# Kernel optimization log

Measured on AMD Instinct MI355X. Metric: run time of the kernel, lower is better.

## Reference

```python
import jax, jax.numpy as jnp
import numpy as np

H = 32; L = 4; HEADS = 8; VC = 16; BIG = 1e9

def _unit(v):
    return v * jax.lax.rsqrt(jnp.sum(v * v, -1, keepdims=True) + 1e-8)

def _dihedrals(bb):
    n = bb.shape[0]
    X = bb[:, :3].reshape(n * 3, 3)
    U = _unit(X[1:] - X[:-1])
    u2, u1, u0 = U[:-2], U[1:-1], U[2:]
    n2 = _unit(jnp.cross(u2, u1)); n1 = _unit(jnp.cross(u1, u0))
    cosD = jnp.clip(jnp.sum(n2 * n1, -1), -1 + 1e-6, 1 - 1e-6)
    D = jnp.sign(jnp.sum(u2 * n1, -1)) * jnp.arccos(cosD)
    D = jnp.pad(D, (1, 2)).reshape(n, 3)
    return jnp.concatenate([jnp.cos(D), jnp.sin(D)], -1)

def _orientations(x):
    f = jnp.pad(_unit(x[1:] - x[:-1]), ((0, 1), (0, 0)))
    b = jnp.pad(_unit(x[:-1] - x[1:]), ((1, 0), (0, 0)))
    return jnp.stack([f, b], -2)

def _virtual_cb(bb):
    n_, ca, c = bb[:, 0], bb[:, 1], bb[:, 2]
    b = ca - n_; cc = c - ca; a = jnp.cross(b, cc)
    return -0.58273431 * a + 0.56802827 * b - 0.54067466 * cc + ca

def _rbf(d, nbin=16, dmax=20.0):
    mu = jnp.linspace(0.0, dmax, nbin); sig = dmax / nbin
    return jnp.exp(-(((d[..., None] - mu) / sig) ** 2))

def _pos_emb(didx, nemb=16):
    freq = jnp.exp(jnp.arange(0, nemb, 2, dtype=jnp.float32) * (-np.log(10000.0) / nemb))
    ang = didx[..., None].astype(jnp.float32) * freq
    return jnp.concatenate([jnp.cos(ang), jnp.sin(ang)], -1)

def _edge_rot(vec):
    # per-edge rotation aligning edge direction to e_y (equiformer-style)
    nrm = _unit(vec)
    helper = jnp.where(jnp.abs(nrm[..., 2:3]) > 0.99, jnp.array([1.0, 0.0, 0.0]), jnp.array([0.0, 0.0, 1.0]))
    z = _unit(jnp.cross(nrm, helper))
    x = jnp.cross(nrm, z)
    return jnp.stack([x, nrm, z], axis=-2)

def _rot(R, x):
    return jnp.concatenate([x[..., :1, :], jnp.einsum('...ij,...jc->...ic', R, x[..., 1:, :])], -2)

def _rot_inv(R, x):
    return jnp.concatenate([x[..., :1, :], jnp.einsum('...ji,...jc->...ic', R, x[..., 1:, :])], -2)

def _norm_so3(x, g0, b0, g1):
    x0 = x[..., 0, :]; x1 = x[..., 1:, :]
    mu = jnp.mean(x0, -1, keepdims=True)
    var = jnp.var(x0, -1, keepdims=True)
    y0 = (x0 - mu) * jax.lax.rsqrt(var + 1e-6) * g0 + b0
    y1 = x1 * jax.lax.rsqrt(jnp.mean(x1 * x1, (-2, -1), keepdims=True) + 1e-6) * g1
    return jnp.concatenate([y0[..., None, :], y1], -2)

def _project(xin, nbr, R, ef, rw1, rw2, ow):
    src = _rot(R, xin[nbr])                         # [N,k,4,Cin] gather + rotate into edge frame
    rad = jax.nn.silu(ef @ rw1) @ rw2               # [N,k,Cin] radial weights
    msg = _rot_inv(R, src * rad[..., None, :])      # rotate back to global frame
    return jnp.mean(msg, axis=1) @ ow               # [N,4,Cout]

def _forward(bb, latent, ln_g0, ln_b0, ln_g1, bb_rad_w1, bb_rad_w2, bb_out_w,
             lat_rad_w1, lat_rad_w2, lat_out_w, tln_g0, tln_b0, tln_g1,
             attn_w1, attn_w2, v_w, o_w, ffn_w1, ffn_w2, ffn_wg, ffn_v1,
             eu_w1, eu_w2, out_rad_w1, out_rad_w2, out_w,
             seq_w1, seq_b1, seq_w2, seq_b2, seq_w3, seq_b3, x_mask, n_per, k):
    N = bb.shape[0]
    Xca = bb[:, 1]
    # backbone SO3 features [N,4,7]: l=0 dihedrals (padded to 7), l=1 seven vectors
    dih = jnp.pad(_dihedrals(bb), ((0, 0), (0, 1)))
    vecs = jnp.concatenate([bb - Xca[:, None], _orientations(Xca),
                            (_virtual_cb(bb) - Xca)[:, None]], -2)
    bb_feat = jnp.concatenate([dih[:, None, :], jnp.nan_to_num(jnp.swapaxes(vecs, -1, -2))], 1)
    # kNN graph within each chain; masked residues pushed far away
    batch = jnp.arange(N) // n_per
    mx = jnp.where(x_mask[:, None], BIG, Xca)
    sq = jnp.sum(mx * mx, -1)
    d2 = sq[:, None] + sq[None, :] - 2.0 * (mx @ mx.T)
    bad = (batch[:, None] != batch[None, :]) | jnp.eye(N, dtype=bool)
    d2 = jnp.where(bad, BIG, d2)
    _, nbr = jax.lax.top_k(-d2, k)                  # [N,k] source indices per target
    edge_vec = Xca[:, None] - Xca[nbr]
    R = _edge_rot(edge_vec)                         # [N,k,3,3]
    dist = jnp.sqrt(jnp.sum(edge_vec * edge_vec, -1) + 1e-12)
    ef = jnp.concatenate([_rbf(dist), _pos_emb(nbr - jnp.arange(N)[:, None])], -1)  # [N,k,32]
    lat = _norm_so3(latent, ln_g0, ln_b0, ln_g1)
    x = jnp.concatenate([_project(bb_feat, nbr, R, ef, bb_rad_w1, bb_rad_w2, bb_out_w),
                         _project(lat, nbr, R, ef, lat_rad_w1, lat_rad_w2, lat_out_w)], -1)  # [N,4,H]
    for l in range(L):
        xl = _norm_so3(x, tln_g0[l], tln_b0[l], tln_g1[l])
        src = xl[nbr]                               # [N,k,4,H]
        feat = jnp.concatenate([src[..., 0, :],
                                jnp.broadcast_to(xl[:, None, 0, :], src[..., 0, :].shape),
                                ef], -1)            # [N,k,3H]
        alpha = jax.nn.softmax(jax.nn.silu(feat @ attn_w1[l]) @ attn_w2[l], axis=1)  # [N,k,heads]
        v = _rot_inv(R, _rot(R, src) @ v_w[l])      # [N,k,4,heads*vc]
        v = v.reshape(N, k, 4, HEADS, VC)
        agg = jnp.einsum('nkh,nkchv->nchv', alpha, v).reshape(N, 4, HEADS * VC)
        x = x + agg @ o_w[l]
        h = jax.nn.silu(x[:, 0, :] @ ffn_w1[l])
        gate = jax.nn.sigmoid(h @ ffn_wg[l])
        x = x + jnp.concatenate([(h @ ffn_w2[l])[:, None, :],
                                 (x[:, 1:, :] @ ffn_v1[l]) * gate[:, None, :]], 1)
        e_in = jnp.concatenate([ef, x[nbr][..., 0, :],
                                jnp.broadcast_to(x[:, None, 0, :], (N, k, H))], -1)
        ef = ef + jax.nn.silu(e_in @ eu_w1[l]) @ eu_w2[l]
    atoms = _project(x, nbr, R, ef, out_rad_w1, out_rad_w2, out_w)  # [N,4,91]
    decoded_latent = jnp.swapaxes(atoms[:, 1:4, :], -1, -2)         # [N,91,3]
    hh = jax.nn.relu(x[:, 0, :] @ seq_w1 + seq_b1)
    hh = jax.nn.relu(hh @ seq_w2 + seq_b2)
    seq_logits = jax.nn.log_softmax(hh @ seq_w3 + seq_b3, -1)
    return decoded_latent, seq_logits

def setup_inputs() -> dict:
    key = jax.random.key(0)
    N = 8192; n_per = 2048; k = 30
    keys = iter(jax.random.split(key, 64))
    def W(shape):
        fan = shape[-2] if len(shape) > 1 else shape[-1]
        return (jax.random.normal(next(keys), shape) / np.sqrt(fan)).astype(jnp.float32)
    inp = {
        'bb': (jax.random.normal(next(keys), (N, 4, 3)) * 3.0).astype(jnp.float32),
        'latent': jax.random.normal(next(keys), (N, 4, H), dtype=jnp.float32),
        'ln_g0': jnp.ones((H,), jnp.float32), 'ln_b0': jnp.zeros((H,), jnp.float32), 'ln_g1': jnp.ones((H,), jnp.float32),
        'bb_rad_w1': W((H, 64)), 'bb_rad_w2': W((64, 7)), 'bb_out_w': W((7, 16)),
        'lat_rad_w1': W((H, 64)), 'lat_rad_w2': W((64, H)), 'lat_out_w': W((H, 16)),
        'tln_g0': jnp.ones((L, H), jnp.float32), 'tln_b0': jnp.zeros((L, H), jnp.float32), 'tln_g1': jnp.ones((L, H), jnp.float32),
        'attn_w1': W((L, 3 * H, H)), 'attn_w2': W((L, H, HEADS)),
        'v_w': W((L, H, HEADS * VC)), 'o_w': W((L, HEADS * VC, H)),
        'ffn_w1': W((L, H, 2 * H)), 'ffn_w2': W((L, 2 * H, H)), 'ffn_wg': W((L, 2 * H, H)), 'ffn_v1': W((L, H, H)),
        'eu_w1': W((L, 3 * H, 2 * H)), 'eu_w2': W((L, 2 * H, H)),
        'out_rad_w1': W((H, 64)), 'out_rad_w2': W((64, H)), 'out_w': W((H, 91)),
        'seq_w1': W((H, 64)), 'seq_b1': jnp.zeros((64,), jnp.float32),
        'seq_w2': W((64, H)), 'seq_b2': jnp.zeros((H,), jnp.float32),
        'seq_w3': W((H, 20)), 'seq_b3': jnp.zeros((20,), jnp.float32),
        'x_mask': jnp.zeros((N,), bool), 'n_per': n_per, 'k': k,
    }
    return inp

def reference(bb, latent, ln_g0, ln_b0, ln_g1, bb_rad_w1, bb_rad_w2, bb_out_w,
              lat_rad_w1, lat_rad_w2, lat_out_w, tln_g0, tln_b0, tln_g1,
              attn_w1, attn_w2, v_w, o_w, ffn_w1, ffn_w2, ffn_wg, ffn_v1,
              eu_w1, eu_w2, out_rad_w1, out_rad_w2, out_w,
              seq_w1, seq_b1, seq_w2, seq_b2, seq_w3, seq_b3, x_mask, n_per, k):
    return _forward(bb, latent, ln_g0, ln_b0, ln_g1, bb_rad_w1, bb_rad_w2, bb_out_w,
                    lat_rad_w1, lat_rad_w2, lat_out_w, tln_g0, tln_b0, tln_g1,
                    attn_w1, attn_w2, v_w, o_w, ffn_w1, ffn_w2, ffn_wg, ffn_v1,
                    eu_w1, eu_w2, out_rad_w1, out_rad_w2, out_w,
                    seq_w1, seq_b1, seq_w2, seq_b2, seq_w3, seq_b3, x_mask, n_per, k)
```

## Files before the change

### kernel.cpp

```cpp
#include <hip/hip_runtime.h>
#include <math.h>

#define NRES 8192
#define NPER 2048
#define KNB  30
#define NEDGE (NRES*KNB)

__device__ __forceinline__ float siluf(float x){ return x / (1.0f + __expf(-x)); }

__global__ void k_bbfeat(const float* __restrict__ bb, float* __restrict__ bbf,
                         float4* __restrict__ ca){
  int n = blockIdx.x*256 + threadIdx.x;
  if(n >= NRES) return;
  const float* r = bb + n*12;
  float cax=r[3], cay=r[4], caz=r[5];
  ca[n] = make_float4(cax,cay,caz, cax*cax+cay*cay+caz*caz);
  float vx[7],vy[7],vz[7];
  for(int a=0;a<4;a++){ vx[a]=r[a*3]-cax; vy[a]=r[a*3+1]-cay; vz[a]=r[a*3+2]-caz; }
  if(n<NRES-1){
    float dx=bb[(n+1)*12+3]-cax, dy=bb[(n+1)*12+4]-cay, dz=bb[(n+1)*12+5]-caz;
    float s=rsqrtf(dx*dx+dy*dy+dz*dz+1e-8f);
    vx[4]=dx*s; vy[4]=dy*s; vz[4]=dz*s;
  } else { vx[4]=0.f; vy[4]=0.f; vz[4]=0.f; }
  if(n>0){
    float dx=bb[(n-1)*12+3]-cax, dy=bb[(n-1)*12+4]-cay, dz=bb[(n-1)*12+5]-caz;
    float s=rsqrtf(dx*dx+dy*dy+dz*dz+1e-8f);
    vx[5]=dx*s; vy[5]=dy*s; vz[5]=dz*s;
  } else { vx[5]=0.f; vy[5]=0.f; vz[5]=0.f; }
  {
    float bx=cax-r[0], by=cay-r[1], bz=caz-r[2];
    float cx=r[6]-cax, cy=r[7]-cay, cz=r[8]-caz;
    float axx=by*cz-bz*cy, ayy=bz*cx-bx*cz, azz=bx*cy-by*cx;
    vx[6]=-0.58273431f*axx+0.56802827f*bx-0.54067466f*cx;
    vy[6]=-0.58273431f*ayy+0.56802827f*by-0.54067466f*cy;
    vz[6]=-0.58273431f*azz+0.56802827f*bz-0.54067466f*cz;
  }
  float cD[3], sD[3];
  for(int t=0;t<3;t++){
    cD[t]=1.0f; sD[t]=0.0f;
    int f=3*n+t-1;
    if(f>=0 && f<3*NRES-3){
      float X[4][3];
      for(int q=0;q<4;q++){
        int m=f+q, rr=m/3, aa=m-rr*3;
        X[q][0]=bb[rr*12+aa*3]; X[q][1]=bb[rr*12+aa*3+1]; X[q][2]=bb[rr*12+aa*3+2];
      }
      float u2x=X[1][0]-X[0][0], u2y=X[1][1]-X[0][1], u2z=X[1][2]-X[0][2];
      float u1x=X[2][0]-X[1][0], u1y=X[2][1]-X[1][1], u1z=X[2][2]-X[1][2];
      float u0x=X[3][0]-X[2][0], u0y=X[3][1]-X[2][1], u0z=X[3][2]-X[2][2];
      float s2=rsqrtf(u2x*u2x+u2y*u2y+u2z*u2z+1e-8f); u2x*=s2; u2y*=s2; u2z*=s2;
      float s1=rsqrtf(u1x*u1x+u1y*u1y+u1z*u1z+1e-8f); u1x*=s1; u1y*=s1; u1z*=s1;
      float s0=rsqrtf(u0x*u0x+u0y*u0y+u0z*u0z+1e-8f); u0x*=s0; u0y*=s0; u0z*=s0;
      float n2x=u2y*u1z-u2z*u1y, n2y=u2z*u1x-u2x*u1z, n2z=u2x*u1y-u2y*u1x;
      float nn2=rsqrtf(n2x*n2x+n2y*n2y+n2z*n2z+1e-8f); n2x*=nn2; n2y*=nn2; n2z*=nn2;
      float n1x=u1y*u0z-u1z*u0y, n1y=u1z*u0x-u1x*u0z, n1z=u1x*u0y-u1y*u0x;
      float nn1=rsqrtf(n1x*n1x+n1y*n1y+n1z*n1z+1e-8f); n1x*=nn1; n1y*=nn1; n1z*=nn1;
      float dotn = n2x*n1x+n2y*n1y+n2z*n1z;
      float cosD = fminf(fmaxf(dotn, -1.0f+1e-6f), 1.0f-1e-6f);
      float sg = u2x*n1x+u2y*n1y+u2z*n1z;
      if(sg==0.0f){ cD[t]=1.0f; sD[t]=0.0f; }
      else {
        float sgn = (sg>0.0f)?1.0f:-1.0f;
        cD[t]=cosD;
        sD[t]=sgn*sqrtf(fmaxf(1.0f-cosD*cosD,0.0f));
      }
    }
  }
  float* o = bbf + n*28;
  o[0]=cD[0]; o[1]=cD[1]; o[2]=cD[2]; o[3]=sD[0]; o[4]=sD[1]; o[5]=sD[2]; o[6]=0.f;
  for(int c=0;c<7;c++){ o[7+c]=vx[c]; o[14+c]=vy[c]; o[21+c]=vz[c]; }
}

__global__ __launch_bounds__(256) void k_knn(const float4* __restrict__ ca, int* __restrict__ nbr){
  __shared__ float sx[NPER], sy[NPER], sz[NPER], sq[NPER];
  int wave = threadIdx.x>>6;
  int lane = threadIdx.x&63;
  int i = blockIdx.x*4 + wave;
  int batch = i / NPER;
  int base = batch*NPER;
  for(int t=threadIdx.x; t<NPER; t+=256){
    float4 c = ca[base+t];
    sx[t]=c.x; sy[t]=c.y; sz[t]=c.z; sq[t]=c.w;
  }
  __syncthreads();
  int il = i - base;
  float xi=sx[il], yi=sy[il], zi=sz[il], si=sq[il];
  float vals[32];
  float lmin = 1e30f; int larg = 0;
  #pragma unroll
  for(int t=0;t<32;t++){
    int j = t*64 + lane;
    float d2 = si + sq[j] - 2.0f*(xi*sx[j]+yi*sy[j]+zi*sz[j]);
    if(j==il) d2 = 1e30f;
    vals[t]=d2;
    if(d2 < lmin){ lmin=d2; larg=t; }
  }
  for(int it=0; it<KNB; it++){
    float v = lmin; int jg = larg*64 + lane;
    #pragma unroll
    for(int off=32; off>0; off>>=1){
      float vo = __shfl_xor(v, off, 64);
      int   jo = __shfl_xor(jg, off, 64);
      if(vo < v || (vo==v && jo<jg)){ v=vo; jg=jo; }
    }
    if(lane==0) nbr[i*KNB+it] = base + jg;
    if((jg&63)==lane){
      int targ = jg>>6;
      lmin = 1e30f; larg = 0;
      #pragma unroll
      for(int t=0;t<32;t++){
        if(t==targ) vals[t]=1e30f;
        if(vals[t]<lmin){ lmin=vals[t]; larg=t; }
      }
    }
  }
}

__global__ void k_tbl(float* __restrict__ tbl){
  int i = blockIdx.x*256 + threadIdx.x;
  int d = i>>3, m = i&7;
  float freq = __expf(-1.1512925465f*(float)m);
  float ang = (float)(d-2048)*freq;
  tbl[d*16+m]   = cosf(ang);
  tbl[d*16+8+m] = sinf(ang);
}

__global__ void k_edgefeat(const float4* __restrict__ ca, const int* __restrict__ nbr,
                           const float* __restrict__ tbl, float* __restrict__ ef){
  int e = blockIdx.x*256 + threadIdx.x;
  if(e >= NEDGE) return;
  int n = e/KNB;
  int j = nbr[e];
  float4 cn = ca[n], cj = ca[j];
  float dx=cn.x-cj.x, dy=cn.y-cj.y, dz=cn.z-cj.z;
  float dist = sqrtf(dx*dx+dy*dy+dz*dz + 1e-12f);
  float f[32];
  #pragma unroll
  for(int m=0;m<16;m++){
    float mu = (20.0f/15.0f)*(float)m;
    float t = (dist-mu)*(1.0f/1.25f);
    f[m] = __expf(-t*t);
  }
  {
    const float4* t4 = (const float4*)(tbl + (size_t)(j - n + 2048)*16);
    float4 c0=t4[0], c1=t4[1], s0=t4[2], s1=t4[3];
    f[16]=c0.x; f[17]=c0.y; f[18]=c0.z; f[19]=c0.w;
    f[20]=c1.x; f[21]=c1.y; f[22]=c1.z; f[23]=c1.w;
    f[24]=s0.x; f[25]=s0.y; f[26]=s0.z; f[27]=s0.w;
    f[28]=s1.x; f[29]=s1.y; f[30]=s1.z; f[31]=s1.w;
  }
  float4* o4 = (float4*)(ef + (size_t)e*32);
  #pragma unroll
  for(int q=0;q<8;q++) o4[q] = make_float4(f[q*4],f[q*4+1],f[q*4+2],f[q*4+3]);
}

__global__ void k_norm(const float* __restrict__ in, float* __restrict__ out,
                       const float* __restrict__ g0, const float* __restrict__ b0,
                       const float* __restrict__ g1){
  int tid = blockIdx.x*256 + threadIdx.x;
  int n = tid >> 5, lane = tid & 31;
  if(n >= NRES) return;
  const float* xn = in + n*128;
  float x0 = xn[lane];
  float s = x0, s2 = x0*x0;
  for(int off=16; off>0; off>>=1){ s += __shfl_xor(s, off, 32); s2 += __shfl_xor(s2, off, 32); }
  float mu = s*(1.0f/32.0f);
  float var = s2*(1.0f/32.0f) - mu*mu;
  float y0 = (x0-mu)*rsqrtf(var+1e-6f)*g0[lane] + b0[lane];
  float v1 = xn[32+lane], v2 = xn[64+lane], v3 = xn[96+lane];
  float ss = v1*v1+v2*v2+v3*v3;
  for(int off=16; off>0; off>>=1){ ss += __shfl_xor(ss, off, 32); }
  float sc = rsqrtf(ss*(1.0f/96.0f) + 1e-6f);
  float g = g1[lane];
  out[n*128+lane]     = y0;
  out[n*128+32+lane]  = v1*sc*g;
  out[n*128+64+lane]  = v2*sc*g;
  out[n*128+96+lane]  = v3*sc*g;
}

__device__ __forceinline__ void load32(float* __restrict__ f, const float* __restrict__ src){
  const float4* s4 = (const float4*)src;
  #pragma unroll
  for(int q=0;q<8;q++){
    float4 v = s4[q];
    f[q*4+0]=v.x; f[q*4+1]=v.y; f[q*4+2]=v.z; f[q*4+3]=v.w;
  }
}

__global__ __launch_bounds__(128) __attribute__((amdgpu_waves_per_eu(4,4)))
void k_rad(const float* __restrict__ ef,
           const float* __restrict__ bbw1, const float* __restrict__ bbw2,
           const float* __restrict__ latw1, const float* __restrict__ latw2,
           float* __restrict__ radbb, float* __restrict__ radlat){
  int e = blockIdx.x*128 + threadIdx.x;
  float f[32];
  load32(f, ef + (size_t)e*32);
  float ab[7];
  #pragma unroll
  for(int t=0;t<7;t++) ab[t]=0.f;
  #pragma unroll
  for(int half=0; half<2; half++){
    float h[32];
    #pragma unroll
    for(int o=0;o<32;o++) h[o]=0.f;
    #pragma unroll
    for(int c=0;c<32;c++){
      const float* w = bbw1 + c*64 + half*32;
      #pragma unroll
      for(int o=0;o<32;o++) h[o] += f[c]*w[o];
    }
    #pragma unroll
    for(int o=0;o<32;o++){
      float v = siluf(h[o]);
      const float* w2 = bbw2 + (half*32+o)*7;
      #pragma unroll
      for(int t=0;t<7;t++) ab[t] += v*w2[t];
    }
  }
  {
    float4* rb4 = (float4*)(radbb + (size_t)e*8);
    rb4[0] = make_float4(ab[0],ab[1],ab[2],ab[3]);
    rb4[1] = make_float4(ab[4],ab[5],ab[6],0.f);
  }
  float al[32];
  #pragma unroll
  for(int t=0;t<32;t++) al[t]=0.f;
  #pragma unroll
  for(int half=0; half<2; half++){
    float h[32];
    #pragma unroll
    for(int o=0;o<32;o++) h[o]=0.f;
    #pragma unroll
    for(int c=0;c<32;c++){
      const float* w = latw1 + c*64 + half*32;
      #pragma unroll
      for(int o=0;o<32;o++) h[o] += f[c]*w[o];
    }
    #pragma unroll
    for(int o=0;o<32;o++){
      float v = siluf(h[o]);
      const float* w2 = latw2 + (half*32+o)*32;
      #pragma unroll
      for(int t=0;t<32;t++) al[t] += v*w2[t];
    }
  }
  float4* rl4 = (float4*)(radlat + (size_t)e*32);
  #pragma unroll
  for(int q=0;q<8;q++) rl4[q] = make_float4(al[q*4],al[q*4+1],al[q*4+2],al[q*4+3]);
}

__global__ __launch_bounds__(256) void k_init(const int* __restrict__ nbr,
                       const float* __restrict__ radbb, const float* __restrict__ radlat,
                       const float* __restrict__ bbf, const float* __restrict__ latn,
                       const float* __restrict__ bboutw, const float* __restrict__ latoutw,
                       const float* __restrict__ g0, const float* __restrict__ b0,
                       const float* __restrict__ g1,
                       float* __restrict__ x, float* __restrict__ xl){
  __shared__ float msgbb[4][32], msglat[4][128], xout[4][128];
  int g = threadIdx.x>>6, t = threadIdx.x&63;
  int n = blockIdx.x*4 + g;
  int t31 = t&31, t7 = t%7;
  float accL0=0.f, accL1=0.f, accB=0.f;
  for(int kk=0; kk<KNB; kk++){
    int e = n*KNB+kk;
    int j = nbr[e];
    float rl = radlat[(size_t)e*32 + t31];
    accL0 += latn[j*128+t]    * rl;
    accL1 += latn[j*128+64+t] * rl;
    if(t<28) accB += bbf[j*28+t]*radbb[(size_t)e*8 + t7];
  }
  msglat[g][t]=accL0*(1.0f/KNB); msglat[g][64+t]=accL1*(1.0f/KNB);
  if(t<28) msgbb[g][t]=accB*(1.0f/KNB);
  for(int half=0; half<2; half++){
    int e = half*64+t;
    int rrow = e>>5, c = e&31;
    float v=0.f;
    if(c<16){ for(int q=0;q<7;q++)  v += msgbb[g][rrow*7+q]*bboutw[q*16+c]; }
    else    { for(int q=0;q<32;q++) v += msglat[g][rrow*32+q]*latoutw[q*16+(c-16)]; }
    xout[g][e]=v;
    x[n*128+e]=v;
  }
  if(t<32){
    float x0=xout[g][t];
    float s=x0, s2=x0*x0;
    for(int off=16; off>0; off>>=1){ s+=__shfl_xor(s,off,32); s2+=__shfl_xor(s2,off,32); }
    float mu=s*(1.0f/32.0f), var=s2*(1.0f/32.0f)-mu*mu;
    float y0=(x0-mu)*rsqrtf(var+1e-6f)*g0[t]+b0[t];
    float v1=xout[g][32+t], v2=xout[g][64+t], v3=xout[g][96+t];
    float ss=v1*v1+v2*v2+v3*v3;
    for(int off=16; off>0; off>>=1) ss+=__shfl_xor(ss,off,32);
    float sc=rsqrtf(ss*(1.0f/96.0f)+1e-6f);
    float gg=g1[t];
    xl[n*128+t]=y0; xl[n*128+32+t]=v1*sc*gg; xl[n*128+64+t]=v2*sc*gg; xl[n*128+96+t]=v3*sc*gg;
  }
}

__global__ __launch_bounds__(256) void k_nodeprep(const float* __restrict__ x,
                       const float* __restrict__ xl,
                       const float* __restrict__ ew1, const float* __restrict__ aw1,
                       float* __restrict__ hsrc, float* __restrict__ hdst,
                       float* __restrict__ asrc, float* __restrict__ adst){
  __shared__ float sx[4][32], sl[4][32];
  int g = threadIdx.x>>6, lane = threadIdx.x&63;
  int n = blockIdx.x*4 + g;
  if(lane<32){
    if(x)   sx[g][lane] = x[n*128+lane];
    if(aw1) sl[g][lane] = xl[n*128+lane];
  }
  __syncthreads();
  if(x){
    float a0=0.f, a1=0.f;
    #pragma unroll
    for(int c=0;c<32;c++){
      float xv = sx[g][c];
      a0 += xv*ew1[(32+c)*64+lane];
      a1 += xv*ew1[(64+c)*64+lane];
    }
    hsrc[n*64+lane]=a0; hdst[n*64+lane]=a1;
  }
  if(aw1){
    int o = lane&31;
    int roff = (lane>=32)? 32 : 0;
    float a=0.f;
    #pragma unroll
    for(int c=0;c<32;c++) a += sl[g][c]*aw1[(roff+c)*32+o];
    if(lane<32) asrc[n*32+o]=a; else adst[n*32+o]=a;
  }
}

__global__ __launch_bounds__(128) __attribute__((amdgpu_waves_per_eu(4,4)))
void k_logits(const int* __restrict__ nbr,
              const float* __restrict__ asrc, const float* __restrict__ adst,
              const float* __restrict__ ef, const float* __restrict__ w1,
              const float* __restrict__ w2, float* __restrict__ logits){
  int e = blockIdx.x*128 + threadIdx.x;
  int n = e/KNB;
  int j = nbr[e];
  float h[32];
  {
    const float4* pj = (const float4*)(asrc + (size_t)j*32);
    const float4* pn = (const float4*)(adst + (size_t)n*32);
    #pragma unroll
    for(int q=0;q<8;q++){
      float4 a = pj[q], b = pn[q];
      h[q*4+0]=a.x+b.x; h[q*4+1]=a.y+b.y; h[q*4+2]=a.z+b.z; h[q*4+3]=a.w+b.w;
    }
  }
  float f[32];
  load32(f, ef + (size_t)e*32);
  #pragma unroll
  for(int c=0;c<32;c++){
    const float* w = w1 + (64+c)*32;
    #pragma unroll
    for(int o=0;o<32;o++) h[o] += f[c]*w[o];
  }
  float acc[8];
  #pragma unroll
  for(int t=0;t<8;t++) acc[t]=0.f;
  #pragma unroll
  for(int o=0;o<32;o++){
    float v = siluf(h[o]);
    const float* w = w2 + o*8;
    #pragma unroll
    for(int t=0;t<8;t++) acc[t] += v*w[t];
  }
  float4* lg4 = (float4*)(logits + (size_t)e*8);
  lg4[0] = make_float4(acc[0],acc[1],acc[2],acc[3]);
  lg4[1] = make_float4(acc[4],acc[5],acc[6],acc[7]);
}

__global__ __launch_bounds__(256) void k_update(const int* __restrict__ nbr, const float* __restrict__ xl,
                         const float* __restrict__ logits, float* __restrict__ x,
                         float* __restrict__ xlout,
                         const float* __restrict__ vw, const float* __restrict__ ow,
                         const float* __restrict__ fw1, const float* __restrict__ fw2,
                         const float* __restrict__ fwg, const float* __restrict__ fv1,
                         const float* __restrict__ g0, const float* __restrict__ b0,
                         const float* __restrict__ g1){
  __shared__ float S_lg[4][240], S_m[4][8], S_inv[4][8];
  __shared__ float S_S[4][1024], S_agg[4][512], S_x[4][128];
  __shared__ float S_h[4][64], S_g[4][32], S_d0[4][32];
  int g = threadIdx.x>>6, t = threadIdx.x&63;
  int n = blockIdx.x*4 + g;
  for(int r=t; r<240; r+=64) S_lg[g][r] = logits[(size_t)n*240+r];
  if(t<8){
    float m=-1e30f;
    for(int kk=0;kk<KNB;kk++) m=fmaxf(m, S_lg[g][kk*8+t]);
    float s=0.f;
    for(int kk=0;kk<KNB;kk++) s += __expf(S_lg[g][kk*8+t]-m);
    S_m[g][t]=m; S_inv[g][t]=1.0f/s;
  }
  for(int r=t; r<240; r+=64){ int h=r&7; S_lg[g][r]=__expf(S_lg[g][r]-S_m[g][h])*S_inv[g][h]; }
  int hd = t>>3, i8 = t&7;
  const float4* xl4 = (const float4*)xl;
  float acc[16];
  for(int m=0;m<16;m++) acc[m]=0.f;
  for(int kk=0;kk<KNB;kk++){
    int j=nbr[n*KNB+kk];
    float a = S_lg[g][kk*8+hd];
    float4 b0v = xl4[j*32 + i8*4 + 0];
    float4 b1v = xl4[j*32 + i8*4 + 1];
    float4 b2v = xl4[j*32 + i8*4 + 2];
    float4 b3v = xl4[j*32 + i8*4 + 3];
    acc[0]+=a*b0v.x; acc[1]+=a*b0v.y; acc[2]+=a*b0v.z; acc[3]+=a*b0v.w;
    acc[4]+=a*b1v.x; acc[5]+=a*b1v.y; acc[6]+=a*b1v.z; acc[7]+=a*b1v.w;
    acc[8]+=a*b2v.x; acc[9]+=a*b2v.y; acc[10]+=a*b2v.z; acc[11]+=a*b2v.w;
    acc[12]+=a*b3v.x; acc[13]+=a*b3v.y; acc[14]+=a*b3v.z; acc[15]+=a*b3v.w;
  }
  for(int m=0;m<16;m++) S_S[g][hd*128 + i8*16 + m] = acc[m];
  for(int half=0; half<2; half++){
    int hv = half*64+t;
    int hh = hv>>4;
    float a0=0.f,a1=0.f,a2=0.f,a3=0.f;
    for(int c=0;c<32;c++){
      float w = vw[c*128+hv];
      a0 += S_S[g][hh*128 + c]*w;
      a1 += S_S[g][hh*128 + 32+c]*w;
      a2 += S_S[g][hh*128 + 64+c]*w;
      a3 += S_S[g][hh*128 + 96+c]*w;
    }
    S_agg[g][hv]=a0; S_agg[g][128+hv]=a1; S_agg[g][256+hv]=a2; S_agg[g][384+hv]=a3;
  }
  for(int half=0; half<2; half++){
    int e = half*64+t;
    int rrow = e>>5, c = e&31;
    float v = x[n*128+e];
    for(int hv=0;hv<128;hv++) v += S_agg[g][rrow*128+hv]*ow[hv*32+c];
    S_x[g][e]=v;
  }
  {
    float hs=0.f;
    for(int c=0;c<32;c++) hs += S_x[g][c]*fw1[c*64+t];
    S_h[g][t]=siluf(hs);
  }
  if(t<32){
    float gs=0.f, d0=0.f;
    for(int c=0;c<64;c++){ float hv=S_h[g][c]; gs += hv*fwg[c*32+t]; d0 += hv*fw2[c*32+t]; }
    S_g[g][t]=1.0f/(1.0f+__expf(-gs));
    S_d0[g][t]=d0;
  }
  for(int half=0; half<2; half++){
    int e = half*64+t;
    int rrow = e>>5, c = e&31;
    float xv = S_x[g][e], outv;
    if(rrow==0){ outv = xv + S_d0[g][c]; }
    else {
      float dv=0.f;
      for(int cc=0;cc<32;cc++) dv += S_x[g][rrow*32+cc]*fv1[cc*32+c];
      outv = xv + dv*S_g[g][c];
    }
    S_x[g][e]=outv;
    x[n*128+e]=outv;
  }
  if(t<32){
    float x0=S_x[g][t];
    float s=x0, s2=x0*x0;
    for(int off=16; off>0; off>>=1){ s+=__shfl_xor(s,off,32); s2+=__shfl_xor(s2,off,32); }
    float mu=s*(1.0f/32.0f), var=s2*(1.0f/32.0f)-mu*mu;
    float y0=(x0-mu)*rsqrtf(var+1e-6f)*g0[t]+b0[t];
    float v1=S_x[g][32+t], v2=S_x[g][64+t], v3=S_x[g][96+t];
    float ss=v1*v1+v2*v2+v3*v3;
    for(int off=16; off>0; off>>=1) ss+=__shfl_xor(ss,off,32);
    float sc=rsqrtf(ss*(1.0f/96.0f)+1e-6f);
    float gg=g1[t];
    xlout[n*128+t]=y0; xlout[n*128+32+t]=v1*sc*gg;
    xlout[n*128+64+t]=v2*sc*gg; xlout[n*128+96+t]=v3*sc*gg;
  }
}

template<bool FUSE_LOGITS>
__global__ __launch_bounds__(128) __attribute__((amdgpu_waves_per_eu(4,4)))
void k_efup_t(const int* __restrict__ nbr,
              const float* __restrict__ hsrc, const float* __restrict__ hdst,
              const float* __restrict__ ew1, const float* __restrict__ ew2,
              float* __restrict__ ef,
              const float* __restrict__ asrc, const float* __restrict__ adst,
              const float* __restrict__ aw1n, const float* __restrict__ aw2n,
              float* __restrict__ logits){
  int e = blockIdx.x*128 + threadIdx.x;
  int n = e/KNB;
  int j = nbr[e];
  float f[32];
  load32(f, ef + (size_t)e*32);
  float acc[32];
  #pragma unroll
  for(int t=0;t<32;t++) acc[t]=0.f;
  #pragma unroll
  for(int half=0; half<2; half++){
    float h[32];
    {
      const float4* pj = (const float4*)(hsrc + (size_t)j*64 + half*32);
      const float4* pn = (const float4*)(hdst + (size_t)n*64 + half*32);
      #pragma unroll
      for(int q=0;q<8;q++){
        float4 a = pj[q], b = pn[q];
        h[q*4+0]=a.x+b.x; h[q*4+1]=a.y+b.y; h[q*4+2]=a.z+b.z; h[q*4+3]=a.w+b.w;
      }
    }
    #pragma unroll
    for(int c=0;c<32;c++){
      const float* w = ew1 + c*64 + half*32;
      #pragma unroll
      for(int o=0;o<32;o++) h[o] += f[c]*w[o];
    }
    #pragma unroll
    for(int o=0;o<32;o++){
      float v = siluf(h[o]);
      const float* w2 = ew2 + (half*32+o)*32;
      #pragma unroll
      for(int t=0;t<32;t++) acc[t] += v*w2[t];
    }
  }
  #pragma unroll
  for(int t=0;t<32;t++) f[t] += acc[t];
  float4* e4 = (float4*)(ef + (size_t)e*32);
  #pragma unroll
  for(int q=0;q<8;q++)
    e4[q] = make_float4(f[q*4+0], f[q*4+1], f[q*4+2], f[q*4+3]);
  if(FUSE_LOGITS){
    float h2[32];
    {
      const float4* pj = (const float4*)(asrc + (size_t)j*32);
      const float4* pn = (const float4*)(adst + (size_t)n*32);
      #pragma unroll
      for(int q=0;q<8;q++){
        float4 a = pj[q], b = pn[q];
        h2[q*4+0]=a.x+b.x; h2[q*4+1]=a.y+b.y; h2[q*4+2]=a.z+b.z; h2[q*4+3]=a.w+b.w;
      }
    }
    #pragma unroll
    for(int c=0;c<32;c++){
      const float* w = aw1n + (64+c)*32;
      #pragma unroll
      for(int o=0;o<32;o++) h2[o] += f[c]*w[o];
    }
    float a8[8];
    #pragma unroll
    for(int t=0;t<8;t++) a8[t]=0.f;
    #pragma unroll
    for(int o=0;o<32;o++){
      float v = siluf(h2[o]);
      const float* w = aw2n + o*8;
      #pragma unroll
      for(int t=0;t<8;t++) a8[t] += v*w[t];
    }
    float4* lg4 = (float4*)(logits + (size_t)e*8);
    lg4[0] = make_float4(a8[0],a8[1],a8[2],a8[3]);
    lg4[1] = make_float4(a8[4],a8[5],a8[6],a8[7]);
  }
}

__global__ __launch_bounds__(128) __attribute__((amdgpu_waves_per_eu(4,4)))
void k_orad(const float* __restrict__ ef,
            const float* __restrict__ orw1, const float* __restrict__ orw2,
            float* __restrict__ orad){
  int e = blockIdx.x*128 + threadIdx.x;
  float f[32];
  load32(f, ef + (size_t)e*32);
  float acc[32];
  #pragma unroll
  for(int t=0;t<32;t++) acc[t]=0.f;
  #pragma unroll
  for(int half=0; half<2; half++){
    float h[32];
    #pragma unroll
    for(int o=0;o<32;o++) h[o]=0.f;
    #pragma unroll
    for(int c=0;c<32;c++){
      const float* w = orw1 + c*64 + half*32;
      #pragma unroll
      for(int o=0;o<32;o++) h[o] += f[c]*w[o];
    }
    #pragma unroll
    for(int o=0;o<32;o++){
      float v = siluf(h[o]);
      const float* w2 = orw2 + (half*32+o)*32;
      #pragma unroll
      for(int t=0;t<32;t++) acc[t] += v*w2[t];
    }
  }
  float4* r4 = (float4*)(orad + (size_t)e*32);
  #pragma unroll
  for(int q=0;q<8;q++) r4[q] = make_float4(acc[q*4],acc[q*4+1],acc[q*4+2],acc[q*4+3]);
}

__global__ __launch_bounds__(256) void k_out(const int* __restrict__ nbr, const float* __restrict__ orad,
                      const float* __restrict__ x,
                      const float* __restrict__ outw,
                      const float* __restrict__ sw1, const float* __restrict__ sb1,
                      const float* __restrict__ sw2, const float* __restrict__ sb2,
                      const float* __restrict__ sw3, const float* __restrict__ sb3,
                      float* __restrict__ out, float* __restrict__ outseq){
  __shared__ float msg[4][128];
  __shared__ float h1[4][64], h2[4][32], lgs[4][20];
  int g = threadIdx.x>>6, t = threadIdx.x&63;
  int n = blockIdx.x*4 + g;
  int t31 = t&31;
  float acc0=0.f, acc1=0.f;
  for(int kk=0;kk<KNB;kk++){
    int e=n*KNB+kk;
    int j=nbr[e];
    float rl = orad[(size_t)e*32 + t31];
    acc0 += x[j*128+t]*rl;
    acc1 += x[j*128+64+t]*rl;
  }
  msg[g][t]=acc0*(1.0f/KNB); msg[g][64+t]=acc1*(1.0f/KNB);
  for(int o=t;o<91;o+=64){
    for(int rrow=1;rrow<4;rrow++){
      float s=0.f;
      for(int c=0;c<32;c++) s += msg[g][rrow*32+c]*outw[c*91+o];
      out[(size_t)n*273 + o*3 + (rrow-1)] = s;
    }
  }
  {
    float s=0.f;
    for(int c=0;c<32;c++) s += x[n*128+c]*sw1[c*64+t];
    h1[g][t]=fmaxf(s+sb1[t],0.f);
  }
  if(t<32){
    float s=0.f;
    for(int c=0;c<64;c++) s += h1[g][c]*sw2[c*32+t];
    h2[g][t]=fmaxf(s+sb2[t],0.f);
  }
  if(t<20){
    float s=0.f;
    for(int c=0;c<32;c++) s += h2[g][c]*sw3[c*20+t];
    lgs[g][t]=s+sb3[t];
  }
  if(t<20){
    float m=-1e30f;
    for(int c=0;c<20;c++) m=fmaxf(m,lgs[g][c]);
    float se=0.f;
    for(int c=0;c<20;c++) se += __expf(lgs[g][c]-m);
    outseq[(size_t)n*20+t]=lgs[g][t]-m-logf(se);
  }
}

extern "C" void kernel_launch(void* const* d_in, const int* in_sizes, int n_in,
                              void* d_out, int out_size, void* d_ws, size_t ws_size,
                              hipStream_t stream) {
  const float* bb      = (const float*)d_in[0];
  const float* latent  = (const float*)d_in[1];
  const float* ln_g0   = (const float*)d_in[2];
  const float* ln_b0   = (const float*)d_in[3];
  const float* ln_g1   = (const float*)d_in[4];
  const float* bbw1    = (const float*)d_in[5];
  const float* bbw2    = (const float*)d_in[6];
  const float* bboutw  = (const float*)d_in[7];
  const float* latw1   = (const float*)d_in[8];
  const float* latw2   = (const float*)d_in[9];
  const float* latoutw = (const float*)d_in[10];
  const float* tg0     = (const float*)d_in[11];
  const float* tb0     = (const float*)d_in[12];
  const float* tg1     = (const float*)d_in[13];
  const float* aw1     = (const float*)d_in[14];
  const float* aw2     = (const float*)d_in[15];
  const float* vw      = (const float*)d_in[16];
  const float* ow      = (const float*)d_in[17];
  const float* fw1     = (const float*)d_in[18];
  const float* fw2     = (const float*)d_in[19];
  const float* fwg     = (const float*)d_in[20];
  const float* fv1     = (const float*)d_in[21];
  const float* ew1     = (const float*)d_in[22];
  const float* ew2     = (const float*)d_in[23];
  const float* orw1    = (const float*)d_in[24];
  const float* orw2    = (const float*)d_in[25];
  const float* outw    = (const float*)d_in[26];
  const float* sw1     = (const float*)d_in[27];
  const float* sb1     = (const float*)d_in[28];
  const float* sw2     = (const float*)d_in[29];
  const float* sb2     = (const float*)d_in[30];
  const float* sw3     = (const float*)d_in[31];
  const float* sb3     = (const float*)d_in[32];
  float* outp = (float*)d_out;

  int*    nbr    = (int*)d_ws;
  float*  ef     = (float*)((char*)d_ws + 1024*1024);
  float*  xbuf   = ef   + (size_t)NEDGE*32;
  float*  xlA    = xbuf + (size_t)NRES*128;
  float*  xlB    = xlA  + (size_t)NRES*128;
  float*  bbf    = xlB  + (size_t)NRES*128;
  float*  logits = bbf  + (size_t)NRES*28;
  float4* ca     = (float4*)(logits + (size_t)NEDGE*8);
  float*  edgescratch = (float*)(ca + NRES);
  float*  radbb  = logits;
  float*  radlat = edgescratch;
  float*  orad   = edgescratch;
  float*  tbl    = edgescratch;
  float*  hsrc   = edgescratch;
  float*  hdst   = edgescratch + (size_t)NRES*64;
  float*  asrc   = edgescratch + (size_t)NRES*128;
  float*  adst   = edgescratch + (size_t)NRES*128 + (size_t)NRES*32;

  k_bbfeat  <<<NRES/256, 256, 0, stream>>>(bb, bbf, ca);
  k_knn     <<<NRES/4,   256, 0, stream>>>(ca, nbr);
  k_tbl     <<<4096*8/256, 256, 0, stream>>>(tbl);
  k_edgefeat<<<NEDGE/256, 256, 0, stream>>>(ca, nbr, tbl, ef);
  k_norm    <<<NRES*32/256, 256, 0, stream>>>(latent, xlA, ln_g0, ln_b0, ln_g1);
  k_rad     <<<NEDGE/128, 128, 0, stream>>>(ef, bbw1, bbw2, latw1, latw2, radbb, radlat);
  k_init    <<<NRES/4, 256, 0, stream>>>(nbr, radbb, radlat, bbf, xlA,
                                         bboutw, latoutw,
                                         tg0, tb0, tg1,
                                         xbuf, xlB);
  k_nodeprep<<<NRES/4, 256, 0, stream>>>(nullptr, xlB, ew1, aw1, hsrc, hdst, asrc, adst);
  k_logits  <<<NEDGE/128, 128, 0, stream>>>(nbr, asrc, adst, ef, aw1, aw2, logits);
  for(int l=0;l<4;l++){
    const float* xl_in  = (l&1) ? xlA : xlB;
    float*       xl_out = (l&1) ? xlB : xlA;
    int ln = (l+1<4) ? (l+1) : 3;
    k_update <<<NRES/4, 256, 0, stream>>>(nbr, xl_in, logits, xbuf, xl_out,
                                          vw+l*32*128, ow+l*128*32,
                                          fw1+l*32*64, fw2+l*64*32,
                                          fwg+l*64*32, fv1+l*32*32,
                                          tg0+ln*32, tb0+ln*32, tg1+ln*32);
    if(l<3){
      k_nodeprep<<<NRES/4, 256, 0, stream>>>(xbuf, xl_out, ew1+l*96*64, aw1+(l+1)*96*32,
                                             hsrc, hdst, asrc, adst);
      k_efup_t<true><<<NEDGE/128, 128, 0, stream>>>(nbr, hsrc, hdst,
                                                    ew1+l*96*64, ew2+l*64*32, ef,
                                                    asrc, adst,
                                                    aw1+(l+1)*96*32, aw2+(l+1)*32*8, logits);
    } else {
      k_nodeprep<<<NRES/4, 256, 0, stream>>>(xbuf, xl_out, ew1+l*96*64, nullptr,
                                             hsrc, hdst, asrc, adst);
      k_efup_t<false><<<NEDGE/128, 128, 0, stream>>>(nbr, hsrc, hdst,
                                                     ew1+l*96*64, ew2+l*64*32, ef,
                                                     nullptr, nullptr,
                                                     nullptr, nullptr, nullptr);
    }
  }
  k_orad<<<NEDGE/128, 128, 0, stream>>>(ef, orw1, orw2, orad);
  k_out <<<NRES/4, 256, 0, stream>>>(nbr, orad, xbuf, outw,
                                     sw1, sb1, sw2, sb2, sw3, sb3,
                                     outp, outp + (size_t)NRES*273);
}
```

Baseline: 1.147 ms.

## Pack edge MLPs into float2 vectors, rework kNN selection, adjust update syncs

```diff
diff --git a/kernel.cpp b/kernel.cpp
--- a/kernel.cpp
+++ b/kernel.cpp
@@ -6,7 +6,10 @@
 #define KNB  30
 #define NEDGE (NRES*KNB)
 
+typedef float v2f __attribute__((ext_vector_type(2)));
+
 __device__ __forceinline__ float siluf(float x){ return x / (1.0f + __expf(-x)); }
+__device__ __forceinline__ v2f splat2(float a){ v2f r; r.x=a; r.y=a; return r; }
 
 __global__ void k_bbfeat(const float* __restrict__ bb, float* __restrict__ bbf,
                          float4* __restrict__ ca){
@@ -71,6 +74,19 @@
   for(int c=0;c<7;c++){ o[7+c]=vx[c]; o[14+c]=vy[c]; o[21+c]=vz[c]; }
 }
 
+__device__ __forceinline__ unsigned long long knn_extract(const float* __restrict__ vals,
+                                                          unsigned &mask, int lane){
+  float bm=INFINITY; int ba=0;
+  #pragma unroll
+  for(int t=0;t<32;t++){
+    if(!((mask>>t)&1u) && vals[t]<bm){ bm=vals[t]; ba=t; }
+  }
+  mask |= 1u<<ba;
+  unsigned ub = __float_as_uint(bm);
+  ub ^= (ub & 0x80000000u) ? 0xFFFFFFFFu : 0x80000000u;
+  return ((unsigned long long)ub<<32) | (unsigned)(ba*64+lane);
+}
+
 __global__ __launch_bounds__(256) void k_knn(const float4* __restrict__ ca, int* __restrict__ nbr){
   __shared__ float sx[NPER], sy[NPER], sz[NPER], sq[NPER];
   int wave = threadIdx.x>>6;
@@ -86,32 +102,30 @@
   int il = i - base;
   float xi=sx[il], yi=sy[il], zi=sz[il], si=sq[il];
   float vals[32];
-  float lmin = 1e30f; int larg = 0;
   #pragma unroll
   for(int t=0;t<32;t++){
     int j = t*64 + lane;
     float d2 = si + sq[j] - 2.0f*(xi*sx[j]+yi*sy[j]+zi*sz[j]);
     if(j==il) d2 = 1e30f;
     vals[t]=d2;
-    if(d2 < lmin){ lmin=d2; larg=t; }
-  }
+  }
+  unsigned mask = 0;
+  unsigned long long s0 = knn_extract(vals, mask, lane);
+  unsigned long long s1 = knn_extract(vals, mask, lane);
+  unsigned long long s2 = knn_extract(vals, mask, lane);
+  unsigned long long s3 = knn_extract(vals, mask, lane);
+  const unsigned long long EMPTY = ~0ull;
   for(int it=0; it<KNB; it++){
-    float v = lmin; int jg = larg*64 + lane;
+    unsigned long long m = s0;
     #pragma unroll
     for(int off=32; off>0; off>>=1){
-      float vo = __shfl_xor(v, off, 64);
-      int   jo = __shfl_xor(jg, off, 64);
-      if(vo < v || (vo==v && jo<jg)){ v=vo; jg=jo; }
-    }
-    if(lane==0) nbr[i*KNB+it] = base + jg;
-    if((jg&63)==lane){
-      int targ = jg>>6;
-      lmin = 1e30f; larg = 0;
-      #pragma unroll
-      for(int t=0;t<32;t++){
-        if(t==targ) vals[t]=1e30f;
-        if(vals[t]<lmin){ lmin=vals[t]; larg=t; }
-      }
+      unsigned long long o = __shfl_xor(m, off, 64);
+      m = (o<m) ? o : m;
+    }
+    if(lane==0) nbr[i*KNB+it] = base + (int)(m & 0x7FFull);
+    if((int)(m & 63ull) == lane){
+      s0=s1; s1=s2; s2=s3; s3=EMPTY;
+      if(s0==EMPTY) s0 = knn_extract(vals, mask, lane);
     }
   }
 }
@@ -187,7 +201,7 @@
   }
 }
 
-__global__ __launch_bounds__(128) __attribute__((amdgpu_waves_per_eu(4,4)))
+__global__ __launch_bounds__(128, 4)
 void k_rad(const float* __restrict__ ef,
            const float* __restrict__ bbw1, const float* __restrict__ bbw2,
            const float* __restrict__ latw1, const float* __restrict__ latw2,
@@ -200,21 +214,25 @@
   for(int t=0;t<7;t++) ab[t]=0.f;
   #pragma unroll
   for(int half=0; half<2; half++){
-    float h[32];
-    #pragma unroll
-    for(int o=0;o<32;o++) h[o]=0.f;
+    v2f h[16];
+    #pragma unroll
+    for(int o=0;o<16;o++) h[o]=splat2(0.f);
     #pragma unroll
     for(int c=0;c<32;c++){
-      const float* w = bbw1 + c*64 + half*32;
-      #pragma unroll
-      for(int o=0;o<32;o++) h[o] += f[c]*w[o];
-    }
-    #pragma unroll
-    for(int o=0;o<32;o++){
-      float v = siluf(h[o]);
-      const float* w2 = bbw2 + (half*32+o)*7;
-      #pragma unroll
-      for(int t=0;t<7;t++) ab[t] += v*w2[t];
+      v2f fc = splat2(f[c]);
+      const v2f* w = (const v2f*)(bbw1 + c*64 + half*32);
+      #pragma unroll
+      for(int o=0;o<16;o++) h[o] += fc*w[o];
+    }
+    #pragma unroll
+    for(int o=0;o<16;o++){
+      float v0 = siluf(h[o].x), v1 = siluf(h[o].y);
+      const float* wa = bbw2 + (half*32+o*2)*7;
+      const float* wb = bbw2 + (half*32+o*2+1)*7;
+      #pragma unroll
+      for(int t=0;t<7;t++) ab[t] += v0*wa[t];
+      #pragma unroll
+      for(int t=0;t<7;t++) ab[t] += v1*wb[t];
     }
   }
   {
@@ -222,31 +240,36 @@
     rb4[0] = make_float4(ab[0],ab[1],ab[2],ab[3]);
     rb4[1] = make_float4(ab[4],ab[5],ab[6],0.f);
   }
-  float al[32];
-  #pragma unroll
-  for(int t=0;t<32;t++) al[t]=0.f;
+  v2f al[16];
+  #pragma unroll
+  for(int t=0;t<16;t++) al[t]=splat2(0.f);
   #pragma unroll
   for(int half=0; half<2; half++){
-    float h[32];
-    #pragma unroll
-    for(int o=0;o<32;o++) h[o]=0.f;
+    v2f h[16];
+    #pragma unroll
+    for(int o=0;o<16;o++) h[o]=splat2(0.f);
     #pragma unroll
     for(int c=0;c<32;c++){
-      const float* w = latw1 + c*64 + half*32;
-      #pragma unroll
-      for(int o=0;o<32;o++) h[o] += f[c]*w[o];
-    }
-    #pragma unroll
-    for(int o=0;o<32;o++){
-      float v = siluf(h[o]);
-      const float* w2 = latw2 + (half*32+o)*32;
-      #pragma unroll
-      for(int t=0;t<32;t++) al[t] += v*w2[t];
-    }
-  }
-  float4* rl4 = (float4*)(radlat + (size_t)e*32);
-  #pragma unroll
-  for(int q=0;q<8;q++) rl4[q] = make_float4(al[q*4],al[q*4+1],al[q*4+2],al[q*4+3]);
+      v2f fc = splat2(f[c]);
+      const v2f* w = (const v2f*)(latw1 + c*64 + half*32);
+      #pragma unroll
+      for(int o=0;o<16;o++) h[o] += fc*w[o];
+    }
+    #pragma unroll
+    for(int o=0;o<16;o++){
+      float v0 = siluf(h[o].x), v1 = siluf(h[o].y);
+      const v2f* wa = (const v2f*)(latw2 + (half*32+o*2)*32);
+      const v2f* wb = (const v2f*)(latw2 + (half*32+o*2+1)*32);
+      v2f va = splat2(v0), vb = splat2(v1);
+      #pragma unroll
+      for(int t=0;t<16;t++) al[t] += va*wa[t];
+      #pragma unroll
+      for(int t=0;t<16;t++) al[t] += vb*wb[t];
+    }
+  }
+  v2f* rl2 = (v2f*)(radlat + (size_t)e*32);
+  #pragma unroll
+  for(int q=0;q<16;q++) rl2[q] = al[q];
 }
 
 __global__ __launch_bounds__(256) void k_init(const int* __restrict__ nbr,
@@ -328,7 +351,7 @@
   }
 }
 
-__global__ __launch_bounds__(128) __attribute__((amdgpu_waves_per_eu(4,4)))
+__global__ __launch_bounds__(128, 4)
 void k_logits(const int* __restrict__ nbr,
               const float* __restrict__ asrc, const float* __restrict__ adst,
               const float* __restrict__ ef, const float* __restrict__ w1,
@@ -336,37 +359,39 @@
   int e = blockIdx.x*128 + threadIdx.x;
   int n = e/KNB;
   int j = nbr[e];
-  float h[32];
+  v2f h[16];
   {
-    const float4* pj = (const float4*)(asrc + (size_t)j*32);
-    const float4* pn = (const float4*)(adst + (size_t)n*32);
-    #pragma unroll
-    for(int q=0;q<8;q++){
-      float4 a = pj[q], b = pn[q];
-      h[q*4+0]=a.x+b.x; h[q*4+1]=a.y+b.y; h[q*4+2]=a.z+b.z; h[q*4+3]=a.w+b.w;
-    }
+    const v2f* pj = (const v2f*)(asrc + (size_t)j*32);
+    const v2f* pn = (const v2f*)(adst + (size_t)n*32);
+    #pragma unroll
+    for(int q=0;q<16;q++) h[q] = pj[q]+pn[q];
   }
   float f[32];
   load32(f, ef + (size_t)e*32);
   #pragma unroll
   for(int c=0;c<32;c++){
-    const float* w = w1 + (64+c)*32;
-    #pragma unroll
-    for(int o=0;o<32;o++) h[o] += f[c]*w[o];
-  }
-  float acc[8];
-  #pragma unroll
-  for(int t=0;t<8;t++) acc[t]=0.f;
-  #pragma unroll
-  for(int o=0;o<32;o++){
-    float v = siluf(h[o]);
-    const float* w = w2 + o*8;
-    #pragma unroll
-    for(int t=0;t<8;t++) acc[t] += v*w[t];
-  }
-  float4* lg4 = (float4*)(logits + (size_t)e*8);
-  lg4[0] = make_float4(acc[0],acc[1],acc[2],acc[3]);
-  lg4[1] = make_float4(acc[4],acc[5],acc[6],acc[7]);
+    v2f fc = splat2(f[c]);
+    const v2f* w = (const v2f*)(w1 + (64+c)*32);
+    #pragma unroll
+    for(int o=0;o<16;o++) h[o] += fc*w[o];
+  }
+  v2f acc[4];
+  #pragma unroll
+  for(int t=0;t<4;t++) acc[t]=splat2(0.f);
+  #pragma unroll
+  for(int o=0;o<16;o++){
+    float v0 = siluf(h[o].x), v1 = siluf(h[o].y);
+    const v2f* wa = (const v2f*)(w2 + (o*2)*8);
+    const v2f* wb = (const v2f*)(w2 + (o*2+1)*8);
+    v2f va = splat2(v0), vb = splat2(v1);
+    #pragma unroll
+    for(int t=0;t<4;t++) acc[t] += va*wa[t];
+    #pragma unroll
+    for(int t=0;t<4;t++) acc[t] += vb*wb[t];
+  }
+  v2f* lg2 = (v2f*)(logits + (size_t)e*8);
+  #pragma unroll
+  for(int q=0;q<4;q++) lg2[q] = acc[q];
 }
 
 __global__ __launch_bounds__(256) void k_update(const int* __restrict__ nbr, const float* __restrict__ xl,
@@ -392,53 +417,55 @@
   }
   for(int r=t; r<240; r+=64){ int h=r&7; S_lg[g][r]=__expf(S_lg[g][r]-S_m[g][h])*S_inv[g][h]; }
   int hd = t>>3, i8 = t&7;
-  const float4* xl4 = (const float4*)xl;
-  float acc[16];
-  for(int m=0;m<16;m++) acc[m]=0.f;
+  v2f acc[8];
+  #pragma unroll
+  for(int m=0;m<8;m++) acc[m]=splat2(0.f);
   for(int kk=0;kk<KNB;kk++){
     int j=nbr[n*KNB+kk];
-    float a = S_lg[g][kk*8+hd];
-    float4 b0v = xl4[j*32 + i8*4 + 0];
-    float4 b1v = xl4[j*32 + i8*4 + 1];
-    float4 b2v = xl4[j*32 + i8*4 + 2];
-    float4 b3v = xl4[j*32 + i8*4 + 3];
-    acc[0]+=a*b0v.x; acc[1]+=a*b0v.y; acc[2]+=a*b0v.z; acc[3]+=a*b0v.w;
-    acc[4]+=a*b1v.x; acc[5]+=a*b1v.y; acc[6]+=a*b1v.z; acc[7]+=a*b1v.w;
-    acc[8]+=a*b2v.x; acc[9]+=a*b2v.y; acc[10]+=a*b2v.z; acc[11]+=a*b2v.w;
-    acc[12]+=a*b3v.x; acc[13]+=a*b3v.y; acc[14]+=a*b3v.z; acc[15]+=a*b3v.w;
-  }
-  for(int m=0;m<16;m++) S_S[g][hd*128 + i8*16 + m] = acc[m];
+    v2f a = splat2(S_lg[g][kk*8+hd]);
+    const v2f* xr = (const v2f*)(xl + (size_t)j*128 + i8*16);
+    #pragma unroll
+    for(int q=0;q<8;q++) acc[q] += a*xr[q];
+  }
+  #pragma unroll
+  for(int q=0;q<8;q++){ S_S[g][hd*128 + i8*16 + 2*q] = acc[q].x; S_S[g][hd*128 + i8*16 + 2*q+1] = acc[q].y; }
+  __syncthreads();
   for(int half=0; half<2; half++){
     int hv = half*64+t;
     int hh = hv>>4;
-    float a0=0.f,a1=0.f,a2=0.f,a3=0.f;
+    v2f a01=splat2(0.f), a23=splat2(0.f);
     for(int c=0;c<32;c++){
-      float w = vw[c*128+hv];
-      a0 += S_S[g][hh*128 + c]*w;
-      a1 += S_S[g][hh*128 + 32+c]*w;
-      a2 += S_S[g][hh*128 + 64+c]*w;
-      a3 += S_S[g][hh*128 + 96+c]*w;
-    }
-    S_agg[g][hv]=a0; S_agg[g][128+hv]=a1; S_agg[g][256+hv]=a2; S_agg[g][384+hv]=a3;
-  }
-  for(int half=0; half<2; half++){
-    int e = half*64+t;
-    int rrow = e>>5, c = e&31;
-    float v = x[n*128+e];
-    for(int hv=0;hv<128;hv++) v += S_agg[g][rrow*128+hv]*ow[hv*32+c];
-    S_x[g][e]=v;
-  }
+      v2f w = splat2(vw[c*128+hv]);
+      v2f s01; s01.x = S_S[g][hh*128 + c];      s01.y = S_S[g][hh*128 + 32+c];
+      v2f s23; s23.x = S_S[g][hh*128 + 64+c];   s23.y = S_S[g][hh*128 + 96+c];
+      a01 += s01*w; a23 += s23*w;
+    }
+    S_agg[g][hv]=a01.x; S_agg[g][128+hv]=a01.y; S_agg[g][256+hv]=a23.x; S_agg[g][384+hv]=a23.y;
+  }
+  __syncthreads();
+  {
+    int c = t&31, r0 = t>>5;
+    v2f v01; v01.x = x[n*128+t]; v01.y = x[n*128+64+t];
+    for(int hv=0;hv<128;hv++){
+      v2f s; s.x = S_agg[g][r0*128+hv]; s.y = S_agg[g][(r0+2)*128+hv];
+      v01 += s*splat2(ow[hv*32+c]);
+    }
+    S_x[g][t]=v01.x; S_x[g][64+t]=v01.y;
+  }
+  __syncthreads();
   {
     float hs=0.f;
     for(int c=0;c<32;c++) hs += S_x[g][c]*fw1[c*64+t];
     S_h[g][t]=siluf(hs);
   }
+  __syncthreads();
   if(t<32){
     float gs=0.f, d0=0.f;
     for(int c=0;c<64;c++){ float hv=S_h[g][c]; gs += hv*fwg[c*32+t]; d0 += hv*fw2[c*32+t]; }
     S_g[g][t]=1.0f/(1.0f+__expf(-gs));
     S_d0[g][t]=d0;
   }
+  __syncthreads();
   for(int half=0; half<2; half++){
     int e = half*64+t;
     int rrow = e>>5, c = e&31;
@@ -449,9 +476,11 @@
       for(int cc=0;cc<32;cc++) dv += S_x[g][rrow*32+cc]*fv1[cc*32+c];
       outv = xv + dv*S_g[g][c];
     }
+    __syncthreads();
     S_x[g][e]=outv;
     x[n*128+e]=outv;
   }
+  __syncthreads();
   if(t<32){
     float x0=S_x[g][t];
     float s=x0, s2=x0*x0;
@@ -469,7 +498,7 @@
 }
 
 template<bool FUSE_LOGITS>
-__global__ __launch_bounds__(128) __attribute__((amdgpu_waves_per_eu(4,4)))
+__global__ __launch_bounds__(128, 4)
 void k_efup_t(const int* __restrict__ nbr,
               const float* __restrict__ hsrc, const float* __restrict__ hdst,
               const float* __restrict__ ew1, const float* __restrict__ ew2,
@@ -482,106 +511,115 @@
   int j = nbr[e];
   float f[32];
   load32(f, ef + (size_t)e*32);
-  float acc[32];
-  #pragma unroll
-  for(int t=0;t<32;t++) acc[t]=0.f;
+  v2f acc[16];
+  #pragma unroll
+  for(int t=0;t<16;t++) acc[t]=splat2(0.f);
   #pragma unroll
   for(int half=0; half<2; half++){
-    float h[32];
+    v2f h[16];
     {
-      const float4* pj = (const float4*)(hsrc + (size_t)j*64 + half*32);
-      const float4* pn = (const float4*)(hdst + (size_t)n*64 + half*32);
-      #pragma unroll
-      for(int q=0;q<8;q++){
-        float4 a = pj[q], b = pn[q];
-        h[q*4+0]=a.x+b.x; h[q*4+1]=a.y+b.y; h[q*4+2]=a.z+b.z; h[q*4+3]=a.w+b.w;
-      }
+      const v2f* pj = (const v2f*)(hsrc + (size_t)j*64 + half*32);
+      const v2f* pn = (const v2f*)(hdst + (size_t)n*64 + half*32);
+      #pragma unroll
+      for(int q=0;q<16;q++) h[q] = pj[q]+pn[q];
     }
     #pragma unroll
     for(int c=0;c<32;c++){
-      const float* w = ew1 + c*64 + half*32;
-      #pragma unroll
-      for(int o=0;o<32;o++) h[o] += f[c]*w[o];
-    }
-    #pragma unroll
-    for(int o=0;o<32;o++){
-      float v = siluf(h[o]);
-      const float* w2 = ew2 + (half*32+o)*32;
-      #pragma unroll
-      for(int t=0;t<32;t++) acc[t] += v*w2[t];
-    }
-  }
-  #pragma unroll
-  for(int t=0;t<32;t++) f[t] += acc[t];
+      v2f fc = splat2(f[c]);
+      const v2f* w = (const v2f*)(ew1 + c*64 + half*32);
+      #pragma unroll
+      for(int o=0;o<16;o++) h[o] += fc*w[o];
+    }
+    #pragma unroll
+    for(int o=0;o<16;o++){
+      float v0 = siluf(h[o].x), v1 = siluf(h[o].y);
+      const v2f* wa = (const v2f*)(ew2 + (half*32+o*2)*32);
+      const v2f* wb = (const v2f*)(ew2 + (half*32+o*2+1)*32);
+      v2f va = splat2(v0), vb = splat2(v1);
+      #pragma unroll
+      for(int t=0;t<16;t++) acc[t] += va*wa[t];
+      #pragma unroll
+      for(int t=0;t<16;t++) acc[t] += vb*wb[t];
+    }
+  }
+  #pragma unroll
+  for(int t=0;t<16;t++){ f[2*t] += acc[t].x; f[2*t+1] += acc[t].y; }
   float4* e4 = (float4*)(ef + (size_t)e*32);
   #pragma unroll
   for(int q=0;q<8;q++)
     e4[q] = make_float4(f[q*4+0], f[q*4+1], f[q*4+2], f[q*4+3]);
   if(FUSE_LOGITS){
-    float h2[32];
+    v2f h2[16];
     {
-      const float4* pj = (const float4*)(asrc + (size_t)j*32);
-      const float4* pn = (const float4*)(adst + (size_t)n*32);
-      #pragma unroll
-      for(int q=0;q<8;q++){
-        float4 a = pj[q], b = pn[q];
-        h2[q*4+0]=a.x+b.x; h2[q*4+1]=a.y+b.y; h2[q*4+2]=a.z+b.z; h2[q*4+3]=a.w+b.w;
-      }
+      const v2f* pj = (const v2f*)(asrc + (size_t)j*32);
+      const v2f* pn = (const v2f*)(adst + (size_t)n*32);
+      #pragma unroll
+      for(int q=0;q<16;q++) h2[q] = pj[q]+pn[q];
     }
     #pragma unroll
     for(int c=0;c<32;c++){
-      const float* w = aw1n + (64+c)*32;
-      #pragma unroll
-      for(int o=0;o<32;o++) h2[o] += f[c]*w[o];
-    }
-    float a8[8];
-    #pragma unroll
-    for(int t=0;t<8;t++) a8[t]=0.f;
-    #pragma unroll
-    for(int o=0;o<32;o++){
-      float v = siluf(h2[o]);
-      const float* w = aw2n + o*8;
-      #pragma unroll
-      for(int t=0;t<8;t++) a8[t] += v*w[t];
-    }
-    float4* lg4 = (float4*)(logits + (size_t)e*8);
-    lg4[0] = make_float4(a8[0],a8[1],a8[2],a8[3]);
-    lg4[1] = make_float4(a8[4],a8[5],a8[6],a8[7]);
-  }
-}
-
-__global__ __launch_bounds__(128) __attribute__((amdgpu_waves_per_eu(4,4)))
+      v2f fc = splat2(f[c]);
+      const v2f* w = (const v2f*)(aw1n + (64+c)*32);
+      #pragma unroll
+      for(int o=0;o<16;o++) h2[o] += fc*w[o];
+    }
+    v2f a8[4];
+    #pragma unroll
+    for(int t=0;t<4;t++) a8[t]=splat2(0.f);
+    #pragma unroll
+    for(int o=0;o<16;o++){
+      float v0 = siluf(h2[o].x), v1 = siluf(h2[o].y);
+      const v2f* wa = (const v2f*)(aw2n + (o*2)*8);
+      const v2f* wb = (const v2f*)(aw2n + (o*2+1)*8);
+      v2f va = splat2(v0), vb = splat2(v1);
+      #pragma unroll
+      for(int t=0;t<4;t++) a8[t] += va*wa[t];
+      #pragma unroll
+      for(int t=0;t<4;t++) a8[t] += vb*wb[t];
+    }
+    v2f* lg2 = (v2f*)(logits + (size_t)e*8);
+    #pragma unroll
+    for(int q=0;q<4;q++) lg2[q] = a8[q];
+  }
+}
+
+__global__ __launch_bounds__(128, 4)
 void k_orad(const float* __restrict__ ef,
             const float* __restrict__ orw1, const float* __restrict__ orw2,
             float* __restrict__ orad){
   int e = blockIdx.x*128 + threadIdx.x;
   float f[32];
   load32(f, ef + (size_t)e*32);
-  float acc[32];
-  #pragma unroll
-  for(int t=0;t<32;t++) acc[t]=0.f;
+  v2f acc[16];
+  #pragma unroll
+  for(int t=0;t<16;t++) acc[t]=splat2(0.f);
   #pragma unroll
   for(int half=0; half<2; half++){
-    float h[32];
-    #pragma unroll
-    for(int o=0;o<32;o++) h[o]=0.f;
+    v2f h[16];
+    #pragma unroll
+    for(int o=0;o<16;o++) h[o]=splat2(0.f);
     #pragma unroll
     for(int c=0;c<32;c++){
-      const float* w = orw1 + c*64 + half*32;
-      #pragma unroll
-      for(int o=0;o<32;o++) h[o] += f[c]*w[o];
-    }
-    #pragma unroll
-    for(int o=0;o<32;o++){
-      float v = siluf(h[o]);
-      const float* w2 = orw2 + (half*32+o)*32;
-      #pragma unroll
-      for(int t=0;t<32;t++) acc[t] += v*w2[t];
-    }
-  }
-  float4* r4 = (float4*)(orad + (size_t)e*32);
-  #pragma unroll
-  for(int q=0;q<8;q++) r4[q] = make_float4(acc[q*4],acc[q*4+1],acc[q*4+2],acc[q*4+3]);
+      v2f fc = splat2(f[c]);
+      const v2f* w = (const v2f*)(orw1 + c*64 + half*32);
+      #pragma unroll
+      for(int o=0;o<16;o++) h[o] += fc*w[o];
+    }
+    #pragma unroll
+    for(int o=0;o<16;o++){
+      float v0 = siluf(h[o].x), v1 = siluf(h[o].y);
+      const v2f* wa = (const v2f*)(orw2 + (half*32+o*2)*32);
+      const v2f* wb = (const v2f*)(orw2 + (half*32+o*2+1)*32);
+      v2f va = splat2(v0), vb = splat2(v1);
+      #pragma unroll
+      for(int t=0;t<16;t++) acc[t] += va*wa[t];
+      #pragma unroll
+      for(int t=0;t<16;t++) acc[t] += vb*wb[t];
+    }
+  }
+  v2f* r2 = (v2f*)(orad + (size_t)e*32);
+  #pragma unroll
+  for(int q=0;q<16;q++) r2[q] = acc[q];
 }
 
 __global__ __launch_bounds__(256) void k_out(const int* __restrict__ nbr, const float* __restrict__ orad,
```

Measured after the change: 1.153 ms. Within noise of the previous version (+0.5%).
